# Kernel optimization log

Measured on AMD Instinct MI355X. Metric: run time of the kernel, lower is better.

Reference implementation:

```python
import jax, jax.numpy as jnp
import numpy as np

ALPHA = 0.5  # matches init_kwargs alpha
EPS = 1e-6
NUM_CLASSES = 100000
FEAT_DIM = 256
BATCH = 16384


def setup_inputs() -> dict:
    key = jax.random.key(0)
    k1, k2, k3 = jax.random.split(key, 3)
    centers = jax.random.normal(k1, (NUM_CLASSES, FEAT_DIM), dtype=jnp.float32)
    features = jax.random.normal(k2, (BATCH, FEAT_DIM), dtype=jnp.float32)
    target = jax.random.randint(k3, (BATCH,), 0, NUM_CLASSES, dtype=jnp.int64)
    return {"centers": centers, "features": features, "target": target}


def reference(centers, features, target):
    # Gather centers for each sample's label: [B, D]
    centers_batch = centers[target]
    # MSE loss (mean over all elements), same as nn.MSELoss()
    center_loss = jnp.mean(jnp.square(features - centers_batch))
    # Per-sample residual
    diff = centers_batch - features  # [B, D]
    # appear_times[i] = number of samples in batch sharing target[i]
    counts = jnp.zeros((centers.shape[0],), dtype=centers.dtype).at[target].add(1.0)
    appear_times = counts[target][:, None]  # [B, 1]
    # Normalized, scaled update (torch code divides by count + eps, scales by alpha)
    update = (ALPHA * diff) / (appear_times + EPS)
    # Serial loop `centers[target[i]] -= update[i]` == scatter-subtract with accumulation
    new_centers = centers.at[target].add(-update)
    return center_loss, new_centers
```

## Files before the change

### kernel.cpp

```cpp
#include <hip/hip_runtime.h>

#define NUM_CLASSES 100000
#define FEAT_DIM    256
#define BATCH       16384
#define ALPHA       0.5f
#define EPS_        1e-6f

typedef float f4 __attribute__((ext_vector_type(4)));
typedef f4 __attribute__((aligned(4))) f4_u;

#define OFF_COUNTS    0u
#define OFF_HEAD      400000u
#define OFF_NSLOTS    800000u
#define OFF_ZERO_END  800016u
#define OFF_SLOT      OFF_ZERO_END
#define OFF_NEXT      (OFF_SLOT + 400000u)
#define OFF_PART2     (OFF_NEXT + 65536u)

__global__ void zero_kernel(f4* __restrict__ p, int n) {
    int i = blockIdx.x * blockDim.x + threadIdx.x;
    if (i < n) p[i] = (f4){0.f, 0.f, 0.f, 0.f};
}

__global__ void count_slot_kernel(const int* __restrict__ target,
                                  int* __restrict__ counts,
                                  int* __restrict__ head,
                                  int* __restrict__ next,
                                  int* __restrict__ slot_of,
                                  int* __restrict__ nslots) {
    int i = blockIdx.x * blockDim.x + threadIdx.x;
    if (i < BATCH) {
        int t = target[i];
        int old = atomicAdd(&counts[t], 1);
        if (old == 0) slot_of[t] = atomicAdd(nslots, 1);
        int prev = atomicExch(&head[t], i + 1);
        next[i] = prev;
    }
}

__global__ void rewrite_kernel(const float* __restrict__ centers,
                               const float* __restrict__ features,
                               const int*   __restrict__ counts,
                               const int*   __restrict__ head,
                               const int*   __restrict__ next,
                               const int*   __restrict__ slot_of,
                               float*       __restrict__ out_centers,
                               float*       __restrict__ partials2) {
    const int wave = threadIdx.x >> 6;
    const int lane = threadIdx.x & 63;
    const int row = blockIdx.x * 4 + wave;
    if (row >= NUM_CLASSES) return;

    const f4 c = *(const f4*)(centers + (size_t)row * FEAT_DIM + lane * 4);
    const int cnt = counts[row];
    f4_u* dst = (f4_u*)(out_centers + (size_t)row * FEAT_DIM + lane * 4);

    if (cnt == 0) {
        *dst = c;
        return;
    }

    f4 sumf = (f4){0.f, 0.f, 0.f, 0.f};
    float s2 = 0.0f;
    for (int j = head[row]; j != 0; j = next[j - 1]) {
        const f4 f = *(const f4*)(features + (size_t)(j - 1) * FEAT_DIM + lane * 4);
        sumf.x += f.x; sumf.y += f.y; sumf.z += f.z; sumf.w += f.w;
        s2 += f.x*f.x + f.y*f.y + f.z*f.z + f.w*f.w;
    }

    const float fc  = (float)cnt;
    const float inv = ALPHA / (fc + EPS_);
    f4 o;
    o.x = c.x - inv * (fc * c.x - sumf.x);
    o.y = c.y - inv * (fc * c.y - sumf.y);
    o.z = c.z - inv * (fc * c.z - sumf.z);
    o.w = c.w - inv * (fc * c.w - sumf.w);
    *dst = o;

    float red = s2
              + fc * (c.x*c.x + c.y*c.y + c.z*c.z + c.w*c.w)
              - 2.0f * (c.x*sumf.x + c.y*sumf.y + c.z*sumf.z + c.w*sumf.w);
    #pragma unroll
    for (int off = 32; off > 0; off >>= 1)
        red += __shfl_down(red, off, 64);
    if (lane == 0) partials2[slot_of[row]] = red;
}

__global__ void reduce_loss(const float* __restrict__ partials2,
                            const int*   __restrict__ nslots,
                            float* __restrict__ out) {
    const int ns = *nslots;
    float s = 0.0f;
    for (int i = threadIdx.x; i < ns; i += 1024) s += partials2[i];
    #pragma unroll
    for (int off = 32; off > 0; off >>= 1)
        s += __shfl_down(s, off, 64);
    __shared__ float wsum[16];
    const int lane = threadIdx.x & 63;
    const int wid  = threadIdx.x >> 6;
    if (lane == 0) wsum[wid] = s;
    __syncthreads();
    if (threadIdx.x == 0) {
        float tot = 0.0f;
        #pragma unroll
        for (int k = 0; k < 16; ++k) tot += wsum[k];
        out[0] = tot * (1.0f / ((float)BATCH * (float)FEAT_DIM));
    }
}

extern "C" void kernel_launch(void* const* d_in, const int* in_sizes, int n_in,
                              void* d_out, int out_size, void* d_ws, size_t ws_size,
                              hipStream_t stream) {
    const float* centers  = (const float*)d_in[0];
    const float* features = (const float*)d_in[1];
    const int*   target   = (const int*)d_in[2];

    float* out         = (float*)d_out;
    float* out_centers = out + 1;

    char* ws = (char*)d_ws;
    int*   counts    = (int*)(ws + OFF_COUNTS);
    int*   head      = (int*)(ws + OFF_HEAD);
    int*   nslots    = (int*)(ws + OFF_NSLOTS);
    int*   slot_of   = (int*)(ws + OFF_SLOT);
    int*   next      = (int*)(ws + OFF_NEXT);
    float* partials2 = (float*)(ws + OFF_PART2);

    const int nzero = (int)(OFF_ZERO_END / 16u);
    zero_kernel<<<(nzero + 255) / 256, 256, 0, stream>>>((f4*)ws, nzero);

    count_slot_kernel<<<(BATCH + 255) / 256, 256, 0, stream>>>(target, counts, head, next,
                                                               slot_of, nslots);

    rewrite_kernel<<<NUM_CLASSES / 4, 256, 0, stream>>>(centers, features, counts, head,
                                                        next, slot_of, out_centers, partials2);

    reduce_loss<<<1, 1024, 0, stream>>>(partials2, nslots, out);
}
```

Before: 54.96 us.

## Shift center output by one float to make stores 16B-aligned; drop slot atomics

The output buffer is offset by one float for the loss scalar, so row stores were misaligned. Each lane now computes the four floats that land on an aligned 16-byte output slot, which straddle two rows: lane 63 also walks the next row's sample list. A finalize kernel handles the first three elements and the loss. The slot_of/nslots atomics are replaced by per-row partials summed in a two-stage reduction, at the cost of extra linked-list traversal and more launches.

```diff
diff --git a/kernel.cpp b/kernel.cpp
--- a/kernel.cpp
+++ b/kernel.cpp
@@ -11,101 +11,164 @@
 
 #define OFF_COUNTS    0u
 #define OFF_HEAD      400000u
-#define OFF_NSLOTS    800000u
-#define OFF_ZERO_END  800016u
-#define OFF_SLOT      OFF_ZERO_END
-#define OFF_NEXT      (OFF_SLOT + 400000u)
-#define OFF_PART2     (OFF_NEXT + 65536u)
+#define OFF_ZERO_END  800000u
+#define OFF_PARTW     800000u
+#define OFF_NEXT      1200000u
+#define OFF_PART64    1265536u
 
 __global__ void zero_kernel(f4* __restrict__ p, int n) {
     int i = blockIdx.x * blockDim.x + threadIdx.x;
     if (i < n) p[i] = (f4){0.f, 0.f, 0.f, 0.f};
 }
 
-__global__ void count_slot_kernel(const int* __restrict__ target,
-                                  int* __restrict__ counts,
-                                  int* __restrict__ head,
-                                  int* __restrict__ next,
-                                  int* __restrict__ slot_of,
-                                  int* __restrict__ nslots) {
+__global__ void count_kernel(const int* __restrict__ target,
+                             int* __restrict__ counts,
+                             int* __restrict__ head,
+                             int* __restrict__ next) {
     int i = blockIdx.x * blockDim.x + threadIdx.x;
     if (i < BATCH) {
         int t = target[i];
-        int old = atomicAdd(&counts[t], 1);
-        if (old == 0) slot_of[t] = atomicAdd(nslots, 1);
+        atomicAdd(&counts[t], 1);
         int prev = atomicExch(&head[t], i + 1);
         next[i] = prev;
     }
 }
 
-__global__ void rewrite_kernel(const float* __restrict__ centers,
+__global__ __launch_bounds__(256) void rewrite_kernel(
+                               const float* __restrict__ centers,
                                const float* __restrict__ features,
                                const int*   __restrict__ counts,
                                const int*   __restrict__ head,
                                const int*   __restrict__ next,
-                               const int*   __restrict__ slot_of,
-                               float*       __restrict__ out_centers,
-                               float*       __restrict__ partials2) {
-    const int wave = threadIdx.x >> 6;
+                               float*       __restrict__ out,
+                               float*       __restrict__ partw) {
     const int lane = threadIdx.x & 63;
-    const int row = blockIdx.x * 4 + wave;
-    if (row >= NUM_CLASSES) return;
-
-    const f4 c = *(const f4*)(centers + (size_t)row * FEAT_DIM + lane * 4);
+    const int row  = blockIdx.x * 4 + (threadIdx.x >> 6);
+    const bool l63  = (lane == 63);
+    const bool last = (row == NUM_CLASSES - 1);
+
+    int coff = 4 * lane + 3;
+    if (l63 && last) coff = 252;
+    const f4 cq = *(const f4_u*)(centers + (size_t)row * FEAT_DIM + coff);
+
     const int cnt = counts[row];
-    f4_u* dst = (f4_u*)(out_centers + (size_t)row * FEAT_DIM + lane * 4);
-
-    if (cnt == 0) {
-        *dst = c;
-        return;
-    }
-
-    f4 sumf = (f4){0.f, 0.f, 0.f, 0.f};
-    float s2 = 0.0f;
-    for (int j = head[row]; j != 0; j = next[j - 1]) {
-        const f4 f = *(const f4*)(features + (size_t)(j - 1) * FEAT_DIM + lane * 4);
-        sumf.x += f.x; sumf.y += f.y; sumf.z += f.z; sumf.w += f.w;
-        s2 += f.x*f.x + f.y*f.y + f.z*f.z + f.w*f.w;
+    const int rn  = last ? row : row + 1;
+    int cnt1 = counts[rn];
+    if (last) cnt1 = 0;
+
+    float s0 = 0.f, s1 = 0.f, s2 = 0.f, s3 = 0.f, sq = 0.f;
+    if (cnt > 0) {
+        const int foff = l63 ? 252 : coff;
+        for (int j = head[row]; j != 0; j = next[j - 1]) {
+            const f4 f = *(const f4_u*)(features + (size_t)(j - 1) * FEAT_DIM + foff);
+            if (l63) { s0 += f.w; sq += f.w * f.w; }
+            else {
+                s0 += f.x; s1 += f.y; s2 += f.z; s3 += f.w;
+                sq += f.x*f.x + f.y*f.y + f.z*f.z + f.w*f.w;
+            }
+        }
+    }
+    float t1 = 0.f, t2 = 0.f, t3 = 0.f, tq = 0.f;
+    if (l63 && cnt1 > 0) {
+        for (int j = head[rn]; j != 0; j = next[j - 1]) {
+            const f4 g = *(const f4*)(features + (size_t)(j - 1) * FEAT_DIM);
+            t1 += g.x; t2 += g.y; t3 += g.z;
+            tq += g.x*g.x + g.y*g.y + g.z*g.z;
+        }
     }
 
     const float fc  = (float)cnt;
     const float inv = ALPHA / (fc + EPS_);
+    float red = 0.f;
     f4 o;
-    o.x = c.x - inv * (fc * c.x - sumf.x);
-    o.y = c.y - inv * (fc * c.y - sumf.y);
-    o.z = c.z - inv * (fc * c.z - sumf.z);
-    o.w = c.w - inv * (fc * c.w - sumf.w);
-    *dst = o;
-
-    float red = s2
-              + fc * (c.x*c.x + c.y*c.y + c.z*c.z + c.w*c.w)
-              - 2.0f * (c.x*sumf.x + c.y*sumf.y + c.z*sumf.z + c.w*sumf.w);
+    if (!l63) {
+        if (cnt == 0) {
+            o = cq;
+        } else {
+            o.x = cq.x - inv * (fc * cq.x - s0);
+            o.y = cq.y - inv * (fc * cq.y - s1);
+            o.z = cq.z - inv * (fc * cq.z - s2);
+            o.w = cq.w - inv * (fc * cq.w - s3);
+            red = sq + fc * (cq.x*cq.x + cq.y*cq.y + cq.z*cq.z + cq.w*cq.w)
+                     - 2.0f * (cq.x*s0 + cq.y*s1 + cq.z*s2 + cq.w*s3);
+        }
+    } else {
+        const float cA = last ? cq.w : cq.x;
+        float oA = cA;
+        if (cnt > 0) {
+            oA   = cA - inv * (fc * cA - s0);
+            red += sq + fc * cA * cA - 2.0f * cA * s0;
+        }
+        o.x = oA; o.y = cq.y; o.z = cq.z; o.w = cq.w;
+        if (cnt1 > 0) {
+            const float fc1  = (float)cnt1;
+            const float inv1 = ALPHA / (fc1 + EPS_);
+            o.y = cq.y - inv1 * (fc1 * cq.y - t1);
+            o.z = cq.z - inv1 * (fc1 * cq.z - t2);
+            o.w = cq.w - inv1 * (fc1 * cq.w - t3);
+            red += tq + fc1 * (cq.y*cq.y + cq.z*cq.z + cq.w*cq.w)
+                      - 2.0f * (cq.y*t1 + cq.z*t2 + cq.w*t3);
+        }
+    }
+
+    if (!(l63 && last)) {
+        ((f4*)out)[(size_t)64 * row + 1 + lane] = o;
+    } else {
+        out[(size_t)64 * 4 * NUM_CLASSES] = o.x;
+    }
+
     #pragma unroll
     for (int off = 32; off > 0; off >>= 1)
         red += __shfl_down(red, off, 64);
-    if (lane == 0) partials2[slot_of[row]] = red;
-}
-
-__global__ void reduce_loss(const float* __restrict__ partials2,
-                            const int*   __restrict__ nslots,
-                            float* __restrict__ out) {
-    const int ns = *nslots;
-    float s = 0.0f;
-    for (int i = threadIdx.x; i < ns; i += 1024) s += partials2[i];
+    if (lane == 0) partw[row] = red;
+}
+
+__global__ void reduce_stage(const float* __restrict__ partw, float* __restrict__ part64) {
+    float s = 0.f;
+    for (int i = blockIdx.x * 256 + threadIdx.x; i < NUM_CLASSES; i += 64 * 256)
+        s += partw[i];
     #pragma unroll
     for (int off = 32; off > 0; off >>= 1)
         s += __shfl_down(s, off, 64);
-    __shared__ float wsum[16];
+    __shared__ float wsum[4];
     const int lane = threadIdx.x & 63;
     const int wid  = threadIdx.x >> 6;
     if (lane == 0) wsum[wid] = s;
     __syncthreads();
-    if (threadIdx.x == 0) {
-        float tot = 0.0f;
-        #pragma unroll
-        for (int k = 0; k < 16; ++k) tot += wsum[k];
-        out[0] = tot * (1.0f / ((float)BATCH * (float)FEAT_DIM));
-    }
+    if (threadIdx.x == 0)
+        part64[blockIdx.x] = wsum[0] + wsum[1] + wsum[2] + wsum[3];
+}
+
+__global__ void finalize_kernel(const float* __restrict__ part64,
+                                const float* __restrict__ centers,
+                                const float* __restrict__ features,
+                                const int*   __restrict__ counts,
+                                const int*   __restrict__ head,
+                                const int*   __restrict__ next,
+                                float* __restrict__ out) {
+    float acc = 0.f;
+    #pragma unroll
+    for (int k = 0; k < 64; ++k) acc += part64[k];
+
+    const float c0 = centers[0], c1 = centers[1], c2 = centers[2];
+    const int cnt = counts[0];
+    float o0 = c0, o1 = c1, o2 = c2;
+    if (cnt > 0) {
+        float s0 = 0.f, s1 = 0.f, s2 = 0.f, sq = 0.f;
+        for (int j = head[0]; j != 0; j = next[j - 1]) {
+            const float* fb = features + (size_t)(j - 1) * FEAT_DIM;
+            const float f0 = fb[0], f1 = fb[1], f2 = fb[2];
+            s0 += f0; s1 += f1; s2 += f2;
+            sq += f0*f0 + f1*f1 + f2*f2;
+        }
+        const float fc = (float)cnt, inv = ALPHA / (fc + EPS_);
+        o0 = c0 - inv * (fc * c0 - s0);
+        o1 = c1 - inv * (fc * c1 - s1);
+        o2 = c2 - inv * (fc * c2 - s2);
+        acc += sq + fc * (c0*c0 + c1*c1 + c2*c2) - 2.0f * (c0*s0 + c1*s1 + c2*s2);
+    }
+    out[1] = o0; out[2] = o1; out[3] = o2;
+    out[0] = acc * (1.0f / ((float)BATCH * (float)FEAT_DIM));
 }
 
 extern "C" void kernel_launch(void* const* d_in, const int* in_sizes, int n_in,
@@ -115,25 +178,24 @@
     const float* features = (const float*)d_in[1];
     const int*   target   = (const int*)d_in[2];
 
-    float* out         = (float*)d_out;
-    float* out_centers = out + 1;
+    float* out = (float*)d_out;
 
     char* ws = (char*)d_ws;
-    int*   counts    = (int*)(ws + OFF_COUNTS);
-    int*   head      = (int*)(ws + OFF_HEAD);
-    int*   nslots    = (int*)(ws + OFF_NSLOTS);
-    int*   slot_of   = (int*)(ws + OFF_SLOT);
-    int*   next      = (int*)(ws + OFF_NEXT);
-    float* partials2 = (float*)(ws + OFF_PART2);
+    int*   counts  = (int*)(ws + OFF_COUNTS);
+    int*   head    = (int*)(ws + OFF_HEAD);
+    float* partw   = (float*)(ws + OFF_PARTW);
+    int*   next    = (int*)(ws + OFF_NEXT);
+    float* part64  = (float*)(ws + OFF_PART64);
 
     const int nzero = (int)(OFF_ZERO_END / 16u);
     zero_kernel<<<(nzero + 255) / 256, 256, 0, stream>>>((f4*)ws, nzero);
 
-    count_slot_kernel<<<(BATCH + 255) / 256, 256, 0, stream>>>(target, counts, head, next,
-                                                               slot_of, nslots);
+    count_kernel<<<(BATCH + 255) / 256, 256, 0, stream>>>(target, counts, head, next);
 
     rewrite_kernel<<<NUM_CLASSES / 4, 256, 0, stream>>>(centers, features, counts, head,
-                                                        next, slot_of, out_centers, partials2);
-
-    reduce_loss<<<1, 1024, 0, stream>>>(partials2, nslots, out);
-}
+                                                        next, out, partw);
+
+    reduce_stage<<<64, 256, 0, stream>>>(partw, part64);
+
+    finalize_kernel<<<1, 1, 0, stream>>>(part64, centers, features, counts, head, next, out);
+}
```

Result: slower. 56.44 us (+2.7%).
